# Optimization experiments

Hardware: AMD Instinct MI355X
Metric: run time of the kernel (lower is better)

The kernel has to match this reference:

```python
import jax, jax.numpy as jnp
import numpy as np

B, T, V, E, H = 64, 32, 10000, 256, 512


def setup_inputs() -> dict:
    key = jax.random.key(0)
    ks = jax.random.split(key, 16)
    s = 0.1
    return {
        "input_x": jax.random.randint(ks[0], (B, T), 0, V, dtype=jnp.int32),
        "given_num": 16,
        "start_token": jnp.zeros((B,), dtype=jnp.int32),
        "g_embeddings": jax.random.normal(ks[1], (V, E), jnp.float32) * s,
        "Wi": jax.random.normal(ks[2], (E, H), jnp.float32) * s,
        "Ui": jax.random.normal(ks[3], (H, H), jnp.float32) * s,
        "bi": jnp.zeros((H,), jnp.float32),
        "Wf": jax.random.normal(ks[4], (E, H), jnp.float32) * s,
        "Uf": jax.random.normal(ks[5], (H, H), jnp.float32) * s,
        "bf": jnp.zeros((H,), jnp.float32),
        "Wog": jax.random.normal(ks[6], (E, H), jnp.float32) * s,
        "Uog": jax.random.normal(ks[7], (H, H), jnp.float32) * s,
        "bog": jnp.zeros((H,), jnp.float32),
        "Wc": jax.random.normal(ks[8], (E, H), jnp.float32) * s,
        "Uc": jax.random.normal(ks[9], (H, H), jnp.float32) * s,
        "bc": jnp.zeros((H,), jnp.float32),
        "Wo": jax.random.normal(ks[10], (H, V), jnp.float32) * s,
        "bo": jnp.zeros((V,), jnp.float32),
    }


def reference(input_x, given_num, start_token, g_embeddings,
              Wi, Ui, bi, Wf, Uf, bf, Wog, Uog, bog, Wc, Uc, bc, Wo, bo):
    # Faithful jax version of ROLLOUT.generate: teacher-force for t < given_num,
    def lstm_cell(x, h, c):
        i = jax.nn.sigmoid(x @ Wi + h @ Ui + bi)
        f = jax.nn.sigmoid(x @ Wf + h @ Uf + bf)
        o = jax.nn.sigmoid(x @ Wog + h @ Uog + bog)
        c_ = jnp.tanh(x @ Wc + h @ Uc + bc)
        c_new = f * c + i * c_
        return o * jnp.tanh(c_new), c_new

    keys = jax.random.split(jax.random.key(42), T)
    teacher = input_x.T  # [T, B]

    def step(carry, xs):
        x_t, h, c = carry
        t, tok_teacher, k = xs
        h, c = lstm_cell(x_t, h, c)
        logits = h @ Wo + bo  # [B, V]
        sampled = jax.random.categorical(k, logits).astype(jnp.int32)
        token = jnp.where(t < given_num, tok_teacher, sampled)
        x_tp1 = g_embeddings[token]  # [B, E]
        return (x_tp1, h, c), token

    x0 = g_embeddings[start_token]
    h0 = jnp.zeros((B, H), jnp.float32)
    c0 = jnp.zeros((B, H), jnp.float32)
    _, tokens = jax.lax.scan(step, (x0, h0, c0), (jnp.arange(T), teacher, keys))
    return tokens.T  # gen_x: [B, T]
```

## Files before the change

kernel.cpp:

```cpp
#include <hip/hip_runtime.h>
#include <stdint.h>

constexpr int NB = 64;
constexpr int NT = 32;
constexpr int NV = 10000;
constexpr int NE = 256;
constexpr int NH = 512;

constexpr int GIVEN_HOST = 16;

#define PARTITIONABLE 1

__device__ float g_h[2][NH * NB];
__device__ float g_cT[2][NH * NB];
__device__ float g_lp[16 * NH * NB];
__device__ unsigned int g_keys[2 * NT];
__device__ unsigned long long g_slots[NT * NB];


__device__ __forceinline__ unsigned int rotl32(unsigned int x, int n) {
  return (x << n) | (x >> (32 - n));
}

__device__ __forceinline__ void threefry2x32(unsigned int k0, unsigned int k1,
                                             unsigned int x0, unsigned int x1,
                                             unsigned int& o0, unsigned int& o1) {
  unsigned int ks0 = k0, ks1 = k1, ks2 = k0 ^ k1 ^ 0x1BD11BDAu;
  const int R0[4] = {13, 15, 26, 6};
  const int R1[4] = {17, 29, 16, 24};
  x0 += ks0; x1 += ks1;
#pragma unroll
  for (int i = 0; i < 5; ++i) {
#pragma unroll
    for (int j = 0; j < 4; ++j) {
      const int r = ((i & 1) == 0) ? R0[j] : R1[j];
      x0 += x1; x1 = rotl32(x1, r); x1 ^= x0;
    }
    const unsigned int inj0 = (i == 0) ? ks1 : (i == 1) ? ks2 : (i == 2) ? ks0
                              : (i == 3) ? ks1 : ks2;
    const unsigned int inj1 = (i == 0) ? ks2 : (i == 1) ? ks0 : (i == 2) ? ks1
                              : (i == 3) ? ks2 : ks0;
    x0 += inj0;
    x1 += inj1 + (unsigned int)(i + 1);
  }
  o0 = x0; o1 = x1;
}

__device__ __forceinline__ float gumbel_from_bits(unsigned int bits) {
  float u = __uint_as_float((bits >> 9) | 0x3F800000u) - 1.0f;
  u = (u == 0.0f) ? 1.17549435e-38f : u;
  return -logf(-logf(u));
}

__device__ __forceinline__ int decode_tok(unsigned long long pk) {
  return (int)(~(unsigned int)(pk & 0xFFFFFFFFull));
}

__global__ void init_kernel() {
  const int gtid = blockIdx.x * blockDim.x + threadIdx.x;
  const int stride = gridDim.x * blockDim.x;
  if (gtid < NT) {
    unsigned int o0, o1;
#if PARTITIONABLE
    threefry2x32(0u, 42u, 0u, (unsigned int)gtid, o0, o1);
    g_keys[2 * gtid] = o0; g_keys[2 * gtid + 1] = o1;
#else
    threefry2x32(0u, 42u, (unsigned int)gtid, (unsigned int)(gtid + NT), o0, o1);
    g_keys[gtid] = o0; g_keys[gtid + NT] = o1;
#endif
  }
  for (int i = gtid; i < NT * NB; i += stride) g_slots[i] = 0ull;
  for (int i = gtid; i < NH * NB; i += stride) {
    g_h[0][i] = 0.0f;
    g_cT[0][i] = 0.0f;
  }
}

__global__ __launch_bounds__(256) void lstm_part_kernel(
    int t, const int* __restrict__ input_x, const int* __restrict__ given_p,
    const int* __restrict__ start_tok, const float* __restrict__ emb,
    const float* __restrict__ Wi, const float* __restrict__ Ui,
    const float* __restrict__ Wf, const float* __restrict__ Uf,
    const float* __restrict__ Wog, const float* __restrict__ Uog,
    const float* __restrict__ Wc, const float* __restrict__ Uc) {
  __shared__ float as_[192 * 66];
  __shared__ int toksh[NB];
  const int tid = threadIdx.x;
  const int vq = tid & 7;
  const int bl0 = (tid >> 3) * 2;
  const int jx = blockIdx.x;
  const int g = blockIdx.y;
  const int q = blockIdx.z;
  const int j = jx * 32 + vq * 4;
  const float* W = (g == 0) ? Wi : (g == 1) ? Wf : (g == 2) ? Wog : Wc;
  const float* U = (g == 0) ? Ui : (g == 1) ? Uf : (g == 2) ? Uog : Uc;
  const int p_in = t & 1;

  float a00 = 0.f, a01 = 0.f, a02 = 0.f, a03 = 0.f;
  float a10 = 0.f, a11 = 0.f, a12 = 0.f, a13 = 0.f;

  if (q < 2) {
    if (tid < NB) {
      int tok;
      if (t == 0) {
        tok = start_tok[tid];
      } else {
        const int given = *given_p;
        if (t - 1 < given) tok = input_x[tid * NT + (t - 1)];
        else tok = decode_tok(g_slots[(t - 1) * NB + tid]);
      }
      toksh[tid] = tok;
    }
    __syncthreads();
    {
      const int b = tid >> 2, sub = tid & 3;
      const float* erow = emb + (size_t)toksh[b] * NE;
      if (q == 0) {
#pragma unroll
        for (int m = 0; m < 12; ++m) {
          const int s = sub + m * 4;
          const float4 v = *(const float4*)(erow + 4 * s);
          const int r = 4 * s;
          as_[(r + 0) * 66 + b] = v.x; as_[(r + 1) * 66 + b] = v.y;
          as_[(r + 2) * 66 + b] = v.z; as_[(r + 3) * 66 + b] = v.w;
        }
      } else {
#pragma unroll
        for (int m = 0; m < 4; ++m) {
          const int s = sub + m * 4;
          const float4 v = *(const float4*)(erow + 192 + 4 * s);
          const int r = 4 * s;
          as_[(r + 0) * 66 + b] = v.x; as_[(r + 1) * 66 + b] = v.y;
          as_[(r + 2) * 66 + b] = v.z; as_[(r + 3) * 66 + b] = v.w;
        }
        const float* hp = g_h[p_in];
#pragma unroll
        for (int m = 0; m < 8; ++m) {
          const int i4 = tid + m * 256;
          const int k = i4 >> 4, b4 = (i4 & 15) * 4;
          const float4 v = *(const float4*)(hp + (size_t)i4 * 4);
          as_[(64 + k) * 66 + b4 + 0] = v.x; as_[(64 + k) * 66 + b4 + 1] = v.y;
          as_[(64 + k) * 66 + b4 + 2] = v.z; as_[(64 + k) * 66 + b4 + 3] = v.w;
        }
      }
    }
    __syncthreads();
    if (q == 0) {
#pragma unroll 16
      for (int k = 0; k < 192; ++k) {
        const float4 w = *(const float4*)(W + k * NH + j);
        const float2 h2 = *(const float2*)(as_ + k * 66 + bl0);
        a00 = fmaf(h2.x, w.x, a00); a01 = fmaf(h2.x, w.y, a01);
        a02 = fmaf(h2.x, w.z, a02); a03 = fmaf(h2.x, w.w, a03);
        a10 = fmaf(h2.y, w.x, a10); a11 = fmaf(h2.y, w.y, a11);
        a12 = fmaf(h2.y, w.z, a12); a13 = fmaf(h2.y, w.w, a13);
      }
    } else {
#pragma unroll 16
      for (int k = 192; k < 256; ++k) {
        const float4 w = *(const float4*)(W + k * NH + j);
        const float2 h2 = *(const float2*)(as_ + (k - 192) * 66 + bl0);
        a00 = fmaf(h2.x, w.x, a00); a01 = fmaf(h2.x, w.y, a01);
        a02 = fmaf(h2.x, w.z, a02); a03 = fmaf(h2.x, w.w, a03);
        a10 = fmaf(h2.y, w.x, a10); a11 = fmaf(h2.y, w.y, a11);
        a12 = fmaf(h2.y, w.z, a12); a13 = fmaf(h2.y, w.w, a13);
      }
#pragma unroll 16
      for (int k = 256; k < 384; ++k) {
        const float4 w = *(const float4*)(U + (k - NE) * NH + j);
        const float2 h2 = *(const float2*)(as_ + (k - 192) * 66 + bl0);
        a00 = fmaf(h2.x, w.x, a00); a01 = fmaf(h2.x, w.y, a01);
        a02 = fmaf(h2.x, w.z, a02); a03 = fmaf(h2.x, w.w, a03);
        a10 = fmaf(h2.y, w.x, a10); a11 = fmaf(h2.y, w.y, a11);
        a12 = fmaf(h2.y, w.z, a12); a13 = fmaf(h2.y, w.w, a13);
      }
    }
  } else {
    {
      const float4* src = (const float4*)(g_h[p_in] + (q * 192 - NE) * NB);
      float4* dst = (float4*)as_;
#pragma unroll
      for (int i = 0; i < 12; ++i) dst[tid + i * 256] = src[tid + i * 256];
    }
    __syncthreads();
    const int r0 = q * 192;
#pragma unroll 16
    for (int k = r0; k < r0 + 192; ++k) {
      const float4 w = *(const float4*)(U + (k - NE) * NH + j);
      const float2 h2 = *(const float2*)(as_ + (k - r0) * NB + bl0);
      a00 = fmaf(h2.x, w.x, a00); a01 = fmaf(h2.x, w.y, a01);
      a02 = fmaf(h2.x, w.z, a02); a03 = fmaf(h2.x, w.w, a03);
      a10 = fmaf(h2.y, w.x, a10); a11 = fmaf(h2.y, w.y, a11);
      a12 = fmaf(h2.y, w.z, a12); a13 = fmaf(h2.y, w.w, a13);
    }
  }

  const size_t base = ((size_t)(q * 4 + g) * NH + j) * NB + bl0;
  float2 s0; s0.x = a00; s0.y = a10;
  float2 s1; s1.x = a01; s1.y = a11;
  float2 s2; s2.x = a02; s2.y = a12;
  float2 s3; s3.x = a03; s3.y = a13;
  *(float2*)(g_lp + base + 0 * NB) = s0;
  *(float2*)(g_lp + base + 1 * NB) = s1;
  *(float2*)(g_lp + base + 2 * NB) = s2;
  *(float2*)(g_lp + base + 3 * NB) = s3;
}

__global__ __launch_bounds__(256) void lstm_fin_kernel(
    int t, const float* __restrict__ bi, const float* __restrict__ bf,
    const float* __restrict__ bog, const float* __restrict__ bc) {
  const int flat = blockIdx.x * 256 + threadIdx.x;
  const int j = flat >> 6;
  float z[4];
#pragma unroll
  for (int g = 0; g < 4; ++g) {
    const float p0 = g_lp[(size_t)(0 * 4 + g) * NH * NB + flat];
    const float p1 = g_lp[(size_t)(1 * 4 + g) * NH * NB + flat];
    const float p2 = g_lp[(size_t)(2 * 4 + g) * NH * NB + flat];
    const float p3 = g_lp[(size_t)(3 * 4 + g) * NH * NB + flat];
    z[g] = ((p0 + p1) + p2) + p3;
  }
  const float zi = z[0] + bi[j];
  const float zf = z[1] + bf[j];
  const float zo = z[2] + bog[j];
  const float zc = z[3] + bc[j];
  const float iv = 1.0f / (1.0f + expf(-zi));
  const float fv = 1.0f / (1.0f + expf(-zf));
  const float ov = 1.0f / (1.0f + expf(-zo));
  const float cc = tanhf(zc);
  const float cold = g_cT[t & 1][flat];
  const float cn = fv * cold + iv * cc;
  g_cT[(t & 1) ^ 1][flat] = cn;
  g_h[(t & 1) ^ 1][flat] = ov * tanhf(cn);
}

__global__ __launch_bounds__(1024) void logits_kernel(
    int t, const int* __restrict__ given_p, const float* __restrict__ Wo,
    const float* __restrict__ bo) {
  const int given = *given_p;
  if (t < given) return;
  __shared__ float hs[NH * NB];
  __shared__ unsigned long long best[NB];
  const int tid = threadIdx.x;
  const int w = tid >> 8;
  const int lt = tid & 255;
  const int vq = lt & 15;
  const int bq = lt >> 4;
  const int n0 = blockIdx.x * 64;
  const int n = n0 + vq * 4;
  const int nl = (n < NV) ? n : 0;

  if (tid < NB) best[tid] = 0ull;

  {
    const float4* src = (const float4*)g_h[(t & 1) ^ 1];
    float4* dst = (float4*)hs;
#pragma unroll
    for (int i = 0; i < 8; ++i) dst[tid + i * 1024] = src[tid + i * 1024];
  }
  __syncthreads();

  float4 A0 = make_float4(0.f, 0.f, 0.f, 0.f);
  float4 A1 = A0, A2 = A0, A3 = A0;
  {
    const float* wp = Wo + (size_t)(w * 128) * NV + nl;
    const float* hb = hs + (w * 128) * NB + bq * 4;
#pragma unroll 8
    for (int kk = 0; kk < 128; ++kk) {
      const float4 w4 = *(const float4*)(wp + (size_t)kk * NV);
      const float4 h4 = *(const float4*)(hb + kk * NB);
      A0.x = fmaf(h4.x, w4.x, A0.x); A0.y = fmaf(h4.x, w4.y, A0.y);
      A0.z = fmaf(h4.x, w4.z, A0.z); A0.w = fmaf(h4.x, w4.w, A0.w);
      A1.x = fmaf(h4.y, w4.x, A1.x); A1.y = fmaf(h4.y, w4.y, A1.y);
      A1.z = fmaf(h4.y, w4.z, A1.z); A1.w = fmaf(h4.y, w4.w, A1.w);
      A2.x = fmaf(h4.z, w4.x, A2.x); A2.y = fmaf(h4.z, w4.y, A2.y);
      A2.z = fmaf(h4.z, w4.z, A2.z); A2.w = fmaf(h4.z, w4.w, A2.w);
      A3.x = fmaf(h4.w, w4.x, A3.x); A3.y = fmaf(h4.w, w4.y, A3.y);
      A3.z = fmaf(h4.w, w4.z, A3.z); A3.w = fmaf(h4.w, w4.w, A3.w);
    }
  }
  __syncthreads();

  {
    float4* pw = (float4*)(hs + w * 4096 + lt * 16);
    pw[0] = A0; pw[1] = A1; pw[2] = A2; pw[3] = A3;
  }
  __syncthreads();

  const int rb = tid >> 4;
  const int rv0 = (tid & 15) * 4;
  const int vg0 = n0 + rv0;
  if (vg0 < NV) {
    const int pidx = ((tid >> 6) * 16 + (tid & 15)) * 16 + ((tid >> 4) & 3) * 4;
    const float4 p0 = *(const float4*)(hs + 0 * 4096 + pidx);
    const float4 p1 = *(const float4*)(hs + 1 * 4096 + pidx);
    const float4 p2 = *(const float4*)(hs + 2 * 4096 + pidx);
    const float4 p3 = *(const float4*)(hs + 3 * 4096 + pidx);
    const unsigned int key0 = g_keys[2 * t], key1 = g_keys[2 * t + 1];
    const float4 bo4 = *(const float4*)(bo + vg0);
    float lg[4];
    lg[0] = ((p0.x + p1.x) + p2.x) + p3.x + bo4.x;
    lg[1] = ((p0.y + p1.y) + p2.y) + p3.y + bo4.y;
    lg[2] = ((p0.z + p1.z) + p2.z) + p3.z + bo4.z;
    lg[3] = ((p0.w + p1.w) + p2.w) + p3.w + bo4.w;
    unsigned long long bp = 0ull;
#pragma unroll
    for (int jj = 0; jj < 4; ++jj) {
      const int v = vg0 + jj;
      unsigned int u0, u1, bits;
#if PARTITIONABLE
      threefry2x32(key0, key1, 0u, (unsigned int)(rb * NV + v), u0, u1);
      bits = u0 ^ u1;
#else
      const int p = rb * NV + v;
      const unsigned int c = (unsigned int)(p >= (NB / 2) * NV ? p - (NB / 2) * NV : p);
      threefry2x32(key0, key1, c, c + (unsigned int)((NB / 2) * NV), u0, u1);
      bits = (p >= (NB / 2) * NV) ? u1 : u0;
#endif
      const float val = gumbel_from_bits(bits) + lg[jj];
      const unsigned int fb = __float_as_uint(val);
      const unsigned int ord = (fb & 0x80000000u) ? ~fb : (fb | 0x80000000u);
      const unsigned long long pk =
          ((unsigned long long)ord << 32) | (unsigned int)(~v);
      bp = (pk > bp) ? pk : bp;
    }
    atomicMax(&best[rb], bp);
  }
  __syncthreads();
  if (tid < NB) atomicMax(&g_slots[t * NB + tid], best[tid]);
}

__global__ void out_kernel(const int* __restrict__ input_x,
                           const int* __restrict__ given_p,
                           int* __restrict__ out) {
  const int b = threadIdx.x;
  if (b >= NB) return;
  const int given = *given_p;
  for (int t = 0; t < NT; ++t) {
    int tok;
    if (t < given) tok = input_x[b * NT + t];
    else tok = decode_tok(g_slots[t * NB + b]);
    out[b * NT + t] = tok;
  }
}

extern "C" void kernel_launch(void* const* d_in, const int* in_sizes, int n_in,
                              void* d_out, int out_size, void* d_ws, size_t ws_size,
                              hipStream_t stream) {
  const int* input_x = (const int*)d_in[0];
  const int* given_num = (const int*)d_in[1];
  const int* start_tok = (const int*)d_in[2];
  const float* emb = (const float*)d_in[3];
  const float* Wi = (const float*)d_in[4];
  const float* Ui = (const float*)d_in[5];
  const float* bi = (const float*)d_in[6];
  const float* Wf = (const float*)d_in[7];
  const float* Uf = (const float*)d_in[8];
  const float* bf = (const float*)d_in[9];
  const float* Wog = (const float*)d_in[10];
  const float* Uog = (const float*)d_in[11];
  const float* bog = (const float*)d_in[12];
  const float* Wc = (const float*)d_in[13];
  const float* Uc = (const float*)d_in[14];
  const float* bc = (const float*)d_in[15];
  const float* Wo = (const float*)d_in[16];
  const float* bo = (const float*)d_in[17];
  int* out = (int*)d_out;

  init_kernel<<<128, 256, 0, stream>>>();
  for (int t = 0; t < NT; ++t) {
    lstm_part_kernel<<<dim3(16, 4, 4), 256, 0, stream>>>(
        t, input_x, given_num, start_tok, emb, Wi, Ui, Wf, Uf, Wog, Uog, Wc, Uc);
    lstm_fin_kernel<<<128, 256, 0, stream>>>(t, bi, bf, bog, bc);
    if (t >= GIVEN_HOST) {
      logits_kernel<<<dim3((NV + 63) / 64), 1024, 0, stream>>>(t, given_num, Wo, bo);
    }
  }
  out_kernel<<<1, 64, 0, stream>>>(input_x, given_num, out);
}
```

Measured before the change: 925.5 us.

## Fuse LSTM gate partial sums and cell update into one kernel

Merges the split-K gate matmul kernel and the finalize kernel into a single 512-thread kernel per step. Each block handles 4 hidden columns for all four gates and all batch rows, and reduces the partial sums in shared memory instead of through a global scratch buffer. This removes one launch per timestep and the global round trip for the partial sums. In exchange the grid drops from 256 to 128 blocks and each thread now computes a 1x4 tile instead of 2x4, which lowers parallelism and per-thread reuse of the weight loads.

```diff
diff --git a/kernel.cpp b/kernel.cpp
--- a/kernel.cpp
+++ b/kernel.cpp
@@ -13,7 +13,6 @@
 
 __device__ float g_h[2][NH * NB];
 __device__ float g_cT[2][NH * NB];
-__device__ float g_lp[16 * NH * NB];
 __device__ unsigned int g_keys[2 * NT];
 __device__ unsigned long long g_slots[NT * NB];
 
@@ -76,162 +75,181 @@
   }
 }
 
-__global__ __launch_bounds__(256) void lstm_part_kernel(
+__global__ __launch_bounds__(512) void lstm_kernel(
     int t, const int* __restrict__ input_x, const int* __restrict__ given_p,
     const int* __restrict__ start_tok, const float* __restrict__ emb,
     const float* __restrict__ Wi, const float* __restrict__ Ui,
     const float* __restrict__ Wf, const float* __restrict__ Uf,
     const float* __restrict__ Wog, const float* __restrict__ Uog,
-    const float* __restrict__ Wc, const float* __restrict__ Uc) {
-  __shared__ float as_[192 * 66];
+    const float* __restrict__ Wc, const float* __restrict__ Uc,
+    const float* __restrict__ bi, const float* __restrict__ bf,
+    const float* __restrict__ bog, const float* __restrict__ bc) {
+  __shared__ float as0[192 * 66];
+  __shared__ float as1[192 * 64];
   __shared__ int toksh[NB];
   const int tid = threadIdx.x;
-  const int vq = tid & 7;
-  const int bl0 = (tid >> 3) * 2;
+  const int grp = tid >> 8;
+  const int lt = tid & 255;
+  const int gg = lt >> 6;
+  const int b = lt & 63;
   const int jx = blockIdx.x;
-  const int g = blockIdx.y;
-  const int q = blockIdx.z;
-  const int j = jx * 32 + vq * 4;
-  const float* W = (g == 0) ? Wi : (g == 1) ? Wf : (g == 2) ? Wog : Wc;
-  const float* U = (g == 0) ? Ui : (g == 1) ? Uf : (g == 2) ? Uog : Uc;
+  const int j = jx * 4;
+  const float* W = (gg == 0) ? Wi : (gg == 1) ? Wf : (gg == 2) ? Wog : Wc;
+  const float* U = (gg == 0) ? Ui : (gg == 1) ? Uf : (gg == 2) ? Uog : Uc;
   const int p_in = t & 1;
 
-  float a00 = 0.f, a01 = 0.f, a02 = 0.f, a03 = 0.f;
-  float a10 = 0.f, a11 = 0.f, a12 = 0.f, a13 = 0.f;
-
-  if (q < 2) {
-    if (tid < NB) {
-      int tok;
-      if (t == 0) {
-        tok = start_tok[tid];
-      } else {
-        const int given = *given_p;
-        if (t - 1 < given) tok = input_x[tid * NT + (t - 1)];
-        else tok = decode_tok(g_slots[(t - 1) * NB + tid]);
-      }
-      toksh[tid] = tok;
-    }
-    __syncthreads();
-    {
-      const int b = tid >> 2, sub = tid & 3;
-      const float* erow = emb + (size_t)toksh[b] * NE;
-      if (q == 0) {
-#pragma unroll
-        for (int m = 0; m < 12; ++m) {
-          const int s = sub + m * 4;
-          const float4 v = *(const float4*)(erow + 4 * s);
-          const int r = 4 * s;
-          as_[(r + 0) * 66 + b] = v.x; as_[(r + 1) * 66 + b] = v.y;
-          as_[(r + 2) * 66 + b] = v.z; as_[(r + 3) * 66 + b] = v.w;
-        }
-      } else {
-#pragma unroll
-        for (int m = 0; m < 4; ++m) {
-          const int s = sub + m * 4;
-          const float4 v = *(const float4*)(erow + 192 + 4 * s);
-          const int r = 4 * s;
-          as_[(r + 0) * 66 + b] = v.x; as_[(r + 1) * 66 + b] = v.y;
-          as_[(r + 2) * 66 + b] = v.z; as_[(r + 3) * 66 + b] = v.w;
-        }
-        const float* hp = g_h[p_in];
-#pragma unroll
-        for (int m = 0; m < 8; ++m) {
-          const int i4 = tid + m * 256;
-          const int k = i4 >> 4, b4 = (i4 & 15) * 4;
-          const float4 v = *(const float4*)(hp + (size_t)i4 * 4);
-          as_[(64 + k) * 66 + b4 + 0] = v.x; as_[(64 + k) * 66 + b4 + 1] = v.y;
-          as_[(64 + k) * 66 + b4 + 2] = v.z; as_[(64 + k) * 66 + b4 + 3] = v.w;
-        }
-      }
-    }
-    __syncthreads();
-    if (q == 0) {
-#pragma unroll 16
-      for (int k = 0; k < 192; ++k) {
-        const float4 w = *(const float4*)(W + k * NH + j);
-        const float2 h2 = *(const float2*)(as_ + k * 66 + bl0);
-        a00 = fmaf(h2.x, w.x, a00); a01 = fmaf(h2.x, w.y, a01);
-        a02 = fmaf(h2.x, w.z, a02); a03 = fmaf(h2.x, w.w, a03);
-        a10 = fmaf(h2.y, w.x, a10); a11 = fmaf(h2.y, w.y, a11);
-        a12 = fmaf(h2.y, w.z, a12); a13 = fmaf(h2.y, w.w, a13);
-      }
+  if (tid < NB) {
+    int tok;
+    if (t == 0) {
+      tok = start_tok[tid];
     } else {
-#pragma unroll 16
-      for (int k = 192; k < 256; ++k) {
-        const float4 w = *(const float4*)(W + k * NH + j);
-        const float2 h2 = *(const float2*)(as_ + (k - 192) * 66 + bl0);
-        a00 = fmaf(h2.x, w.x, a00); a01 = fmaf(h2.x, w.y, a01);
-        a02 = fmaf(h2.x, w.z, a02); a03 = fmaf(h2.x, w.w, a03);
-        a10 = fmaf(h2.y, w.x, a10); a11 = fmaf(h2.y, w.y, a11);
-        a12 = fmaf(h2.y, w.z, a12); a13 = fmaf(h2.y, w.w, a13);
-      }
-#pragma unroll 16
-      for (int k = 256; k < 384; ++k) {
-        const float4 w = *(const float4*)(U + (k - NE) * NH + j);
-        const float2 h2 = *(const float2*)(as_ + (k - 192) * 66 + bl0);
-        a00 = fmaf(h2.x, w.x, a00); a01 = fmaf(h2.x, w.y, a01);
-        a02 = fmaf(h2.x, w.z, a02); a03 = fmaf(h2.x, w.w, a03);
-        a10 = fmaf(h2.y, w.x, a10); a11 = fmaf(h2.y, w.y, a11);
-        a12 = fmaf(h2.y, w.z, a12); a13 = fmaf(h2.y, w.w, a13);
-      }
-    }
-  } else {
-    {
-      const float4* src = (const float4*)(g_h[p_in] + (q * 192 - NE) * NB);
-      float4* dst = (float4*)as_;
-#pragma unroll
-      for (int i = 0; i < 12; ++i) dst[tid + i * 256] = src[tid + i * 256];
-    }
-    __syncthreads();
-    const int r0 = q * 192;
-#pragma unroll 16
-    for (int k = r0; k < r0 + 192; ++k) {
+      const int given = *given_p;
+      if (t - 1 < given) tok = input_x[tid * NT + (t - 1)];
+      else tok = decode_tok(g_slots[(t - 1) * NB + tid]);
+    }
+    toksh[tid] = tok;
+  }
+  __syncthreads();
+
+  float r0 = 0.f, r1 = 0.f, r2 = 0.f, r3 = 0.f;
+  float q0 = 0.f, q1 = 0.f, q2 = 0.f, q3 = 0.f;
+
+  if (grp == 0) {
+    const int bb = lt >> 2, sub = lt & 3;
+    const float* erow = emb + (size_t)toksh[bb] * NE;
+#pragma unroll
+    for (int m = 0; m < 12; ++m) {
+      const int s = sub + m * 4;
+      const float4 v = *(const float4*)(erow + 4 * s);
+      const int r = 4 * s;
+      as0[(r + 0) * 66 + bb] = v.x; as0[(r + 1) * 66 + bb] = v.y;
+      as0[(r + 2) * 66 + bb] = v.z; as0[(r + 3) * 66 + bb] = v.w;
+    }
+  } else {
+    const float4* src = (const float4*)(g_h[p_in] + (2 * 192 - NE) * NB);
+    float4* dst = (float4*)as1;
+#pragma unroll
+    for (int i = 0; i < 12; ++i) dst[lt + i * 256] = src[lt + i * 256];
+  }
+  __syncthreads();
+
+  if (grp == 0) {
+#pragma unroll 16
+    for (int k = 0; k < 192; ++k) {
+      const float4 w = *(const float4*)(W + k * NH + j);
+      const float h = as0[k * 66 + b];
+      r0 = fmaf(h, w.x, r0); r1 = fmaf(h, w.y, r1);
+      r2 = fmaf(h, w.z, r2); r3 = fmaf(h, w.w, r3);
+    }
+  } else {
+#pragma unroll 16
+    for (int k = 384; k < 576; ++k) {
       const float4 w = *(const float4*)(U + (k - NE) * NH + j);
-      const float2 h2 = *(const float2*)(as_ + (k - r0) * NB + bl0);
-      a00 = fmaf(h2.x, w.x, a00); a01 = fmaf(h2.x, w.y, a01);
-      a02 = fmaf(h2.x, w.z, a02); a03 = fmaf(h2.x, w.w, a03);
-      a10 = fmaf(h2.y, w.x, a10); a11 = fmaf(h2.y, w.y, a11);
-      a12 = fmaf(h2.y, w.z, a12); a13 = fmaf(h2.y, w.w, a13);
-    }
-  }
-
-  const size_t base = ((size_t)(q * 4 + g) * NH + j) * NB + bl0;
-  float2 s0; s0.x = a00; s0.y = a10;
-  float2 s1; s1.x = a01; s1.y = a11;
-  float2 s2; s2.x = a02; s2.y = a12;
-  float2 s3; s3.x = a03; s3.y = a13;
-  *(float2*)(g_lp + base + 0 * NB) = s0;
-  *(float2*)(g_lp + base + 1 * NB) = s1;
-  *(float2*)(g_lp + base + 2 * NB) = s2;
-  *(float2*)(g_lp + base + 3 * NB) = s3;
-}
-
-__global__ __launch_bounds__(256) void lstm_fin_kernel(
-    int t, const float* __restrict__ bi, const float* __restrict__ bf,
-    const float* __restrict__ bog, const float* __restrict__ bc) {
-  const int flat = blockIdx.x * 256 + threadIdx.x;
-  const int j = flat >> 6;
-  float z[4];
-#pragma unroll
-  for (int g = 0; g < 4; ++g) {
-    const float p0 = g_lp[(size_t)(0 * 4 + g) * NH * NB + flat];
-    const float p1 = g_lp[(size_t)(1 * 4 + g) * NH * NB + flat];
-    const float p2 = g_lp[(size_t)(2 * 4 + g) * NH * NB + flat];
-    const float p3 = g_lp[(size_t)(3 * 4 + g) * NH * NB + flat];
-    z[g] = ((p0 + p1) + p2) + p3;
-  }
-  const float zi = z[0] + bi[j];
-  const float zf = z[1] + bf[j];
-  const float zo = z[2] + bog[j];
-  const float zc = z[3] + bc[j];
-  const float iv = 1.0f / (1.0f + expf(-zi));
-  const float fv = 1.0f / (1.0f + expf(-zf));
-  const float ov = 1.0f / (1.0f + expf(-zo));
-  const float cc = tanhf(zc);
-  const float cold = g_cT[t & 1][flat];
-  const float cn = fv * cold + iv * cc;
-  g_cT[(t & 1) ^ 1][flat] = cn;
-  g_h[(t & 1) ^ 1][flat] = ov * tanhf(cn);
+      const float h = as1[(k - 384) * 64 + b];
+      r0 = fmaf(h, w.x, r0); r1 = fmaf(h, w.y, r1);
+      r2 = fmaf(h, w.z, r2); r3 = fmaf(h, w.w, r3);
+    }
+  }
+  __syncthreads();
+
+  if (grp == 0) {
+    const int bb = lt >> 2, sub = lt & 3;
+    const float* erow = emb + (size_t)toksh[bb] * NE;
+#pragma unroll
+    for (int m = 0; m < 4; ++m) {
+      const int s = sub + m * 4;
+      const float4 v = *(const float4*)(erow + 192 + 4 * s);
+      const int r = 4 * s;
+      as0[(r + 0) * 66 + bb] = v.x; as0[(r + 1) * 66 + bb] = v.y;
+      as0[(r + 2) * 66 + bb] = v.z; as0[(r + 3) * 66 + bb] = v.w;
+    }
+    const float* hp = g_h[p_in];
+#pragma unroll
+    for (int m = 0; m < 8; ++m) {
+      const int i4 = lt + m * 256;
+      const int k = i4 >> 4, b4 = (i4 & 15) * 4;
+      const float4 v = *(const float4*)(hp + (size_t)i4 * 4);
+      as0[(64 + k) * 66 + b4 + 0] = v.x; as0[(64 + k) * 66 + b4 + 1] = v.y;
+      as0[(64 + k) * 66 + b4 + 2] = v.z; as0[(64 + k) * 66 + b4 + 3] = v.w;
+    }
+  } else {
+    const float4* src = (const float4*)(g_h[p_in] + (3 * 192 - NE) * NB);
+    float4* dst = (float4*)as1;
+#pragma unroll
+    for (int i = 0; i < 12; ++i) dst[lt + i * 256] = src[lt + i * 256];
+  }
+  __syncthreads();
+
+  if (grp == 0) {
+#pragma unroll 16
+    for (int k = 192; k < 256; ++k) {
+      const float4 w = *(const float4*)(W + k * NH + j);
+      const float h = as0[(k - 192) * 66 + b];
+      q0 = fmaf(h, w.x, q0); q1 = fmaf(h, w.y, q1);
+      q2 = fmaf(h, w.z, q2); q3 = fmaf(h, w.w, q3);
+    }
+#pragma unroll 16
+    for (int k = 256; k < 384; ++k) {
+      const float4 w = *(const float4*)(U + (k - NE) * NH + j);
+      const float h = as0[(k - 192) * 66 + b];
+      q0 = fmaf(h, w.x, q0); q1 = fmaf(h, w.y, q1);
+      q2 = fmaf(h, w.z, q2); q3 = fmaf(h, w.w, q3);
+    }
+    r0 += q0; r1 += q1; r2 += q2; r3 += q3;
+  } else {
+#pragma unroll 16
+    for (int k = 576; k < 768; ++k) {
+      const float4 w = *(const float4*)(U + (k - NE) * NH + j);
+      const float h = as1[(k - 576) * 64 + b];
+      q0 = fmaf(h, w.x, q0); q1 = fmaf(h, w.y, q1);
+      q2 = fmaf(h, w.z, q2); q3 = fmaf(h, w.w, q3);
+    }
+  }
+  __syncthreads();
+
+  if (grp == 0) {
+    as0[(gg * 4 + 0) * 64 + b] = r0;
+    as0[(gg * 4 + 1) * 64 + b] = r1;
+    as0[(gg * 4 + 2) * 64 + b] = r2;
+    as0[(gg * 4 + 3) * 64 + b] = r3;
+  } else {
+    as0[1024 + (gg * 4 + 0) * 64 + b] = r0;
+    as0[1024 + (gg * 4 + 1) * 64 + b] = r1;
+    as0[1024 + (gg * 4 + 2) * 64 + b] = r2;
+    as0[1024 + (gg * 4 + 3) * 64 + b] = r3;
+    as0[2048 + (gg * 4 + 0) * 64 + b] = q0;
+    as0[2048 + (gg * 4 + 1) * 64 + b] = q1;
+    as0[2048 + (gg * 4 + 2) * 64 + b] = q2;
+    as0[2048 + (gg * 4 + 3) * 64 + b] = q3;
+  }
+  __syncthreads();
+
+  if (tid < 256) {
+    const int jl = tid >> 6;
+    const int bb = tid & 63;
+    const int jg = jx * 4 + jl;
+    float z[4];
+#pragma unroll
+    for (int g = 0; g < 4; ++g) {
+      const float p01 = as0[(g * 4 + jl) * 64 + bb];
+      const float p2 = as0[1024 + (g * 4 + jl) * 64 + bb];
+      const float p3 = as0[2048 + (g * 4 + jl) * 64 + bb];
+      z[g] = (p01 + p2) + p3;
+    }
+    const float zi = z[0] + bi[jg];
+    const float zf = z[1] + bf[jg];
+    const float zo = z[2] + bog[jg];
+    const float zc = z[3] + bc[jg];
+    const float iv = 1.0f / (1.0f + expf(-zi));
+    const float fv = 1.0f / (1.0f + expf(-zf));
+    const float ov = 1.0f / (1.0f + expf(-zo));
+    const float cc = tanhf(zc);
+    const int flat = jg * 64 + bb;
+    const float cold = g_cT[t & 1][flat];
+    const float cn = fv * cold + iv * cc;
+    g_cT[(t & 1) ^ 1][flat] = cn;
+    g_h[(t & 1) ^ 1][flat] = ov * tanhf(cn);
+  }
 }
 
 __global__ __launch_bounds__(1024) void logits_kernel(
@@ -369,9 +387,9 @@
 
   init_kernel<<<128, 256, 0, stream>>>();
   for (int t = 0; t < NT; ++t) {
-    lstm_part_kernel<<<dim3(16, 4, 4), 256, 0, stream>>>(
-        t, input_x, given_num, start_tok, emb, Wi, Ui, Wf, Uf, Wog, Uog, Wc, Uc);
-    lstm_fin_kernel<<<128, 256, 0, stream>>>(t, bi, bf, bog, bc);
+    lstm_kernel<<<128, 512, 0, stream>>>(
+        t, input_x, given_num, start_tok, emb, Wi, Ui, Wf, Uf, Wog, Uog, Wc, Uc,
+        bi, bf, bog, bc);
     if (t >= GIVEN_HOST) {
       logits_kernel<<<dim3((NV + 63) / 64), 1024, 0, stream>>>(t, given_num, Wo, bo);
     }
```

Result: slower. 1.383 ms (+49.5%).

## Retile logits kernel to 40-column blocks with 640 threads and warp-0 epilogue

Applied to the files above, without the earlier changes.

Retiles the logits GEMV+sampling kernel so each block covers 40 vocabulary columns with 640 threads (4 K-slices of 160), giving exactly 250 blocks and no wasted tail columns. The K-slice partials are reduced only by the first slice group, which keeps its own accumulators in registers and reads the other three from shared memory. That group then does the bias add, Gumbel sampling and argmax for all 4 batch rows it owns. This removes the tail-padding waste and shrinks the partial-sum traffic. In exchange the RNG/argmax epilogue is concentrated in a quarter of the threads, and 640-thread blocks may change occupancy.

```diff
diff --git a/kernel.cpp b/kernel.cpp
--- a/kernel.cpp
+++ b/kernel.cpp
@@ -234,7 +234,7 @@
   g_h[(t & 1) ^ 1][flat] = ov * tanhf(cn);
 }
 
-__global__ __launch_bounds__(1024) void logits_kernel(
+__global__ __launch_bounds__(640) void logits_kernel(
     int t, const int* __restrict__ given_p, const float* __restrict__ Wo,
     const float* __restrict__ bo) {
   const int given = *given_p;
@@ -242,13 +242,13 @@
   __shared__ float hs[NH * NB];
   __shared__ unsigned long long best[NB];
   const int tid = threadIdx.x;
-  const int w = tid >> 8;
-  const int lt = tid & 255;
-  const int vq = lt & 15;
-  const int bq = lt >> 4;
-  const int n0 = blockIdx.x * 64;
+  const int w = tid / 160;
+  const int lane = tid % 160;
+  const int vq = lane % 10;
+  const int bp = lane / 10;
+  const int n0 = blockIdx.x * 40;
   const int n = n0 + vq * 4;
-  const int nl = (n < NV) ? n : 0;
+  const int b0 = bp * 4;
 
   if (tid < NB) best[tid] = 0ull;
 
@@ -256,15 +256,18 @@
     const float4* src = (const float4*)g_h[(t & 1) ^ 1];
     float4* dst = (float4*)hs;
 #pragma unroll
-    for (int i = 0; i < 8; ++i) dst[tid + i * 1024] = src[tid + i * 1024];
+    for (int i = 0; i < 13; ++i) {
+      const int idx = tid + i * 640;
+      if (idx < NH * NB / 4) dst[idx] = src[idx];
+    }
   }
   __syncthreads();
 
   float4 A0 = make_float4(0.f, 0.f, 0.f, 0.f);
   float4 A1 = A0, A2 = A0, A3 = A0;
   {
-    const float* wp = Wo + (size_t)(w * 128) * NV + nl;
-    const float* hb = hs + (w * 128) * NB + bq * 4;
+    const float* wp = Wo + (size_t)(w * 128) * NV + n;
+    const float* hb = hs + (w * 128) * NB + b0;
 #pragma unroll 8
     for (int kk = 0; kk < 128; ++kk) {
       const float4 w4 = *(const float4*)(wp + (size_t)kk * NV);
@@ -281,50 +284,52 @@
   }
   __syncthreads();
 
-  {
-    float4* pw = (float4*)(hs + w * 4096 + lt * 16);
-    pw[0] = A0; pw[1] = A1; pw[2] = A2; pw[3] = A3;
+  if (w > 0) {
+    float4* pw = (float4*)hs + (size_t)(w - 1) * 2560;
+    pw[0 * 160 + lane] = A0; pw[1 * 160 + lane] = A1;
+    pw[2 * 160 + lane] = A2; pw[3 * 160 + lane] = A3;
   }
   __syncthreads();
 
-  const int rb = tid >> 4;
-  const int rv0 = (tid & 15) * 4;
-  const int vg0 = n0 + rv0;
-  if (vg0 < NV) {
-    const int pidx = ((tid >> 6) * 16 + (tid & 15)) * 16 + ((tid >> 4) & 3) * 4;
-    const float4 p0 = *(const float4*)(hs + 0 * 4096 + pidx);
-    const float4 p1 = *(const float4*)(hs + 1 * 4096 + pidx);
-    const float4 p2 = *(const float4*)(hs + 2 * 4096 + pidx);
-    const float4 p3 = *(const float4*)(hs + 3 * 4096 + pidx);
+  if (w == 0) {
     const unsigned int key0 = g_keys[2 * t], key1 = g_keys[2 * t + 1];
-    const float4 bo4 = *(const float4*)(bo + vg0);
-    float lg[4];
-    lg[0] = ((p0.x + p1.x) + p2.x) + p3.x + bo4.x;
-    lg[1] = ((p0.y + p1.y) + p2.y) + p3.y + bo4.y;
-    lg[2] = ((p0.z + p1.z) + p2.z) + p3.z + bo4.z;
-    lg[3] = ((p0.w + p1.w) + p2.w) + p3.w + bo4.w;
-    unsigned long long bp = 0ull;
-#pragma unroll
-    for (int jj = 0; jj < 4; ++jj) {
-      const int v = vg0 + jj;
-      unsigned int u0, u1, bits;
+    const float4 bo4 = *(const float4*)(bo + n);
+    const float4* ex = (const float4*)hs;
+#pragma unroll
+    for (int bi = 0; bi < 4; ++bi) {
+      const float4 p0 = (bi == 0) ? A0 : (bi == 1) ? A1 : (bi == 2) ? A2 : A3;
+      const float4 p1 = ex[0 * 2560 + bi * 160 + lane];
+      const float4 p2 = ex[1 * 2560 + bi * 160 + lane];
+      const float4 p3 = ex[2 * 2560 + bi * 160 + lane];
+      float lg[4];
+      lg[0] = ((p0.x + p1.x) + p2.x) + p3.x + bo4.x;
+      lg[1] = ((p0.y + p1.y) + p2.y) + p3.y + bo4.y;
+      lg[2] = ((p0.z + p1.z) + p2.z) + p3.z + bo4.z;
+      lg[3] = ((p0.w + p1.w) + p2.w) + p3.w + bo4.w;
+      const int bg = b0 + bi;
+      unsigned long long bp_ = 0ull;
+#pragma unroll
+      for (int jj = 0; jj < 4; ++jj) {
+        const int v = n + jj;
+        unsigned int u0, u1, bits;
 #if PARTITIONABLE
-      threefry2x32(key0, key1, 0u, (unsigned int)(rb * NV + v), u0, u1);
-      bits = u0 ^ u1;
+        threefry2x32(key0, key1, 0u, (unsigned int)(bg * NV + v), u0, u1);
+        bits = u0 ^ u1;
 #else
-      const int p = rb * NV + v;
-      const unsigned int c = (unsigned int)(p >= (NB / 2) * NV ? p - (NB / 2) * NV : p);
-      threefry2x32(key0, key1, c, c + (unsigned int)((NB / 2) * NV), u0, u1);
-      bits = (p >= (NB / 2) * NV) ? u1 : u0;
+        const int p = bg * NV + v;
+        const unsigned int c = (unsigned int)(p >= (NB / 2) * NV ? p - (NB / 2) * NV : p);
+        threefry2x32(key0, key1, c, c + (unsigned int)((NB / 2) * NV), u0, u1);
+        bits = (p >= (NB / 2) * NV) ? u1 : u0;
 #endif
-      const float val = gumbel_from_bits(bits) + lg[jj];
-      const unsigned int fb = __float_as_uint(val);
-      const unsigned int ord = (fb & 0x80000000u) ? ~fb : (fb | 0x80000000u);
-      const unsigned long long pk =
-          ((unsigned long long)ord << 32) | (unsigned int)(~v);
-      bp = (pk > bp) ? pk : bp;
-    }
-    atomicMax(&best[rb], bp);
+        const float val = gumbel_from_bits(bits) + lg[jj];
+        const unsigned int fb = __float_as_uint(val);
+        const unsigned int ord = (fb & 0x80000000u) ? ~fb : (fb | 0x80000000u);
+        const unsigned long long pk =
+            ((unsigned long long)ord << 32) | (unsigned int)(~v);
+        bp_ = (pk > bp_) ? pk : bp_;
+      }
+      atomicMax(&best[bg], bp_);
+    }
   }
   __syncthreads();
   if (tid < NB) atomicMax(&g_slots[t * NB + tid], best[tid]);
@@ -373,7 +378,7 @@
         t, input_x, given_num, start_tok, emb, Wi, Ui, Wf, Uf, Wog, Uog, Wc, Uc);
     lstm_fin_kernel<<<128, 256, 0, stream>>>(t, bi, bf, bog, bc);
     if (t >= GIVEN_HOST) {
-      logits_kernel<<<dim3((NV + 63) / 64), 1024, 0, stream>>>(t, given_num, Wo, bo);
+      logits_kernel<<<250, 640, 0, stream>>>(t, given_num, Wo, bo);
     }
   }
   out_kernel<<<1, 64, 0, stream>>>(input_x, given_num, out);
```

After: 895.5 us. -3.2%, faster.
